# Kernel optimization log

Measured on AMD Instinct MI355X. Metric: run time of the kernel, lower is better.

The kernel has to match this reference:

```python
import jax, jax.numpy as jnp
import numpy as np

LN_EPS = 1e-5

def _cell(x, h, c, Wih, Whh, bih, bhh):
    # PyTorch LSTMCell: gate order i, f, g, o
    z = x @ Wih.T + h @ Whh.T + bih + bhh
    i, f, g, o = jnp.split(z, 4, axis=-1)
    c = jax.nn.sigmoid(f) * c + jax.nn.sigmoid(i) * jnp.tanh(g)
    h = jax.nn.sigmoid(o) * jnp.tanh(c)
    return h, c

def _forward(encoder_inputs, decoder_inputs, enc_Wih, enc_Whh, enc_bih, enc_bhh,
             dec_Wih, dec_Whh, dec_bih, dec_bhh, attn_in_w, attn_in_b,
             attn_out_w, attn_out_b, ln_g, ln_b, out_w, out_b):
    B = encoder_inputs.shape[0]
    H = enc_Whh.shape[1]
    Sd = decoder_inputs.shape[1]
    h0 = jnp.zeros((B, H), encoder_inputs.dtype)
    c0 = jnp.zeros((B, H), encoder_inputs.dtype)

    def enc_step(carry, x_t):
        h, c = _cell(x_t, carry[0], carry[1], enc_Wih, enc_Whh, enc_bih, enc_bhh)
        return (h, c), h

    (h_e, c_e), hs = jax.lax.scan(enc_step, (h0, c0), jnp.swapaxes(encoder_inputs, 0, 1))
    enc_out = jnp.swapaxes(hs, 0, 1)  # [B, Se, H]

    # MultiheadAttention (1 head): precompute K, V once since keys/values are static
    Wq, Wk, Wv = jnp.split(attn_in_w, 3, axis=0)
    bq, bk, bv = jnp.split(attn_in_b, 3)
    K = enc_out @ Wk.T + bk  # [B, Se, H]
    V = enc_out @ Wv.T + bv  # [B, Se, H]
    scale = 1.0 / float(np.sqrt(H))

    def dec_step(carry, _):
        h, c, x = carry
        h, c = _cell(x, h, c, dec_Wih, dec_Whh, dec_bih, dec_bhh)
        q = h @ Wq.T + bq  # [B, H], single query per step
        attn = jax.nn.softmax(jnp.einsum('bh,bsh->bs', q, K) * scale, axis=-1)
        ctx = jnp.einsum('bs,bsh->bh', attn, V) @ attn_out_w.T + attn_out_b
        y = ctx + h  # residual with raw (pre-projection) query, as in the torch code
        mu = jnp.mean(y, axis=-1, keepdims=True)
        var = jnp.mean((y - mu) ** 2, axis=-1, keepdims=True)
        y = (y - mu) * jax.lax.rsqrt(var + LN_EPS) * ln_g + ln_b
        out = y @ out_w.T + out_b  # [B, 1]
        return (h, c, out), out

    init = (h_e, c_e, decoder_inputs[:, 0, :])
    _, outs = jax.lax.scan(dec_step, init, None, length=Sd)
    return jnp.swapaxes(outs, 0, 1)  # [B, Sd, 1]

def setup_inputs():
    key = jax.random.key(0)
    ks = jax.random.split(key, 13)
    B, Se, Sd, H, O = 64, 512, 128, 512, 1
    s = 1.0 / float(np.sqrt(H))
    def p(k, shape, sc):
        return (jax.random.uniform(k, shape, jnp.float32) * 2.0 - 1.0) * sc
    return {
        "encoder_inputs": jax.random.normal(ks[0], (B, Se, 1), jnp.float32),
        "decoder_inputs": jax.random.normal(ks[1], (B, Sd, 1), jnp.float32),
        "enc_Wih": p(ks[2], (4 * H, 1), s), "enc_Whh": p(ks[3], (4 * H, H), s),
        "enc_bih": p(ks[4], (4 * H,), s), "enc_bhh": p(ks[5], (4 * H,), s),
        "dec_Wih": p(ks[6], (4 * H, 1), s), "dec_Whh": p(ks[7], (4 * H, H), s),
        "dec_bih": p(ks[8], (4 * H,), s), "dec_bhh": p(ks[9], (4 * H,), s),
        "attn_in_w": p(ks[10], (3 * H, H), s),
        "attn_in_b": jnp.zeros((3 * H,), jnp.float32),
        "attn_out_w": p(ks[11], (H, H), s),
        "attn_out_b": jnp.zeros((H,), jnp.float32),
        "ln_g": jnp.ones((H,), jnp.float32), "ln_b": jnp.zeros((H,), jnp.float32),
        "out_w": p(ks[12], (O, H), s), "out_b": jnp.zeros((O,), jnp.float32),
    }

def reference(encoder_inputs, decoder_inputs, enc_Wih, enc_Whh, enc_bih, enc_bhh,
              dec_Wih, dec_Whh, dec_bih, dec_bhh, attn_in_w, attn_in_b,
              attn_out_w, attn_out_b, ln_g, ln_b, out_w, out_b):
    return _forward(encoder_inputs, decoder_inputs, enc_Wih, enc_Whh, enc_bih, enc_bhh,
                    dec_Wih, dec_Whh, dec_bih, dec_bhh, attn_in_w, attn_in_b,
                    attn_out_w, attn_out_b, ln_g, ln_b, out_w, out_b)
```

## Files before the change

### kernel.cpp

```cpp
#include <hip/hip_runtime.h>
#include <hip/hip_bf16.h>
#include <stdint.h>


#define HID 512
#define NBAT 64
#define SEQE 512
#define SEQD 128
#define NGRP 4
#define GBAT 16
#define GBLK 64
#define NH 8
#define SCALE 0.04419417382415922f
#define FLS 16

typedef __attribute__((ext_vector_type(8))) short bf16x8;
typedef __attribute__((ext_vector_type(4))) float f32x4;
#define MFMA_B16 __builtin_amdgcn_mfma_f32_16x16x32_bf16

static constexpr size_t OFF_G   = 0;
static constexpr size_t OFF_NM  = OFF_G  + (size_t)HID*HID*4;
static constexpr size_t OFF_M0  = OFF_NM + (size_t)HID*HID*4;
static constexpr size_t OFF_N0  = OFF_M0 + 2048;
static constexpr size_t OFF_WQB = OFF_N0 + 2048;
static constexpr size_t OFF_SC  = OFF_WQB + 2048;
static constexpr size_t OFF_HB  = OFF_SC + 256;
static constexpr size_t OFF_CB  = OFF_HB + (size_t)3*NBAT*HID*4;
static constexpr size_t OFF_EBP = OFF_CB + (size_t)NBAT*HID*4;
static constexpr size_t OFF_MD  = OFF_EBP + (size_t)NBAT*4*HID*4;
static constexpr size_t OFF_KB  = OFF_MD + (size_t)NBAT*4*4;
static constexpr size_t OFF_FLG = OFF_KB + (size_t)NBAT*SEQE*4;
static constexpr size_t OFF_XPK = OFF_FLG + (size_t)3*NGRP*GBLK*FLS*4;
static constexpr size_t OFF_BFK = ((OFF_XPK + 512 + 255) & ~(size_t)255);
static constexpr size_t OFF_BFV = OFF_BFK + (size_t)16*32*64*8*2;
static constexpr size_t OFF_EO  = OFF_BFV + (size_t)16*32*64*8*2;
static constexpr size_t OFF_VT  = OFF_EO + (size_t)NBAT*SEQE*HID*2;

__device__ __forceinline__ float bf2f(uint32_t u) {
  union { float f; uint32_t i; } x; x.i = u << 16; return x.f;
}
__device__ __forceinline__ unsigned short bfbits(float f) {
  __hip_bfloat16 h = __float2bfloat16(f);
  return *(unsigned short*)&h;
}
__device__ __forceinline__ uint32_t splitbf(float f) {
  unsigned short hi = bfbits(f);
  union { uint32_t u; float ff; } c; c.u = (uint32_t)hi << 16;
  unsigned short lo = bfbits(f - c.ff);
  return (uint32_t)hi | ((uint32_t)lo << 16);
}
__device__ __forceinline__ float sigm(float x) { return 1.f / (1.f + __expf(-x)); }

__device__ __forceinline__ void stg(float* p, float v) {
  __hip_atomic_store(p, v, __ATOMIC_RELAXED, __HIP_MEMORY_SCOPE_AGENT);
}
__device__ __forceinline__ void stgu(uint32_t* p, uint32_t v) {
  __hip_atomic_store(p, v, __ATOMIC_RELAXED, __HIP_MEMORY_SCOPE_AGENT);
}
__device__ __forceinline__ void stgi(int* p, int v) {
  __hip_atomic_store(p, v, __ATOMIC_RELAXED, __HIP_MEMORY_SCOPE_AGENT);
}
__device__ __forceinline__ void stg64(unsigned long long* p, unsigned long long v) {
  __hip_atomic_store(p, v, __ATOMIC_RELAXED, __HIP_MEMORY_SCOPE_AGENT);
}
__device__ __forceinline__ float ldg1(const float* p) {
  return __hip_atomic_load((float*)p, __ATOMIC_RELAXED, __HIP_MEMORY_SCOPE_AGENT);
}
__device__ __forceinline__ int ldgi(const int* p) {
  return __hip_atomic_load((int*)p, __ATOMIC_RELAXED, __HIP_MEMORY_SCOPE_AGENT);
}
__device__ __forceinline__ unsigned long long ldg8(const void* p) {
  return __hip_atomic_load((unsigned long long*)p, __ATOMIC_RELAXED, __HIP_MEMORY_SCOPE_AGENT);
}

#define POLL_GE(addr, thr) \
  while (ldgi(addr) < (thr)) __builtin_amdgcn_s_sleep(1);
#define CFENCE() __asm__ __volatile__("" ::: "memory")

__global__ __launch_bounds__(256) void k0_prep(
    const float* __restrict__ aiw, const float* __restrict__ aib,
    const float* __restrict__ aow, const float* __restrict__ aob,
    const float* __restrict__ outw, const float* __restrict__ lng,
    const float* __restrict__ lnb, char* __restrict__ ws) {
  float* Gm = (float*)(ws + OFF_G);
  float* Nm = (float*)(ws + OFF_NM);
  float* m0 = (float*)(ws + OFF_M0);
  float* n0 = (float*)(ws + OFF_N0);
  float* wqb = (float*)(ws + OFF_WQB);
  float* sc = (float*)(ws + OFF_SC);
  const int blk = blockIdx.x, tid = threadIdx.x;
  if (blk == 512) {
    uint32_t* hb = (uint32_t*)(ws + OFF_HB);
    int* fl = (int*)(ws + OFF_FLG);
    unsigned long long* xpk = (unsigned long long*)(ws + OFF_XPK);
    for (int i = tid; i < 3*NBAT*HID; i += 256) hb[i] = 0u;
    for (int i = tid; i < 3*NGRP*GBLK*FLS; i += 256) fl[i] = 0;
    for (int i = tid; i < NBAT; i += 256) xpk[i] = 0ull;
    for (int l = tid; l < HID; l += 256) {
      float s = 0.f;
      for (int i = 0; i < HID; i++) s += aib[i] * aiw[(size_t)(HID + i)*HID + l];
      m0[l] = s;
    }
    for (int l = tid; l < HID; l += 256) {
      float s = 0.f;
      for (int i = 0; i < HID; i++) s += aiw[(size_t)i*HID + l] * aib[HID + i];
      wqb[l] = s;
    }
    for (int j = tid; j < HID; j += 256) {
      float s = aob[j];
      for (int i = 0; i < HID; i++) s += aow[(size_t)j*HID + i] * aib[2*HID + i];
      n0[j] = s;
    }
    __shared__ float red[256];
    float a = 0.f, b = 0.f, d = 0.f;
    for (int l = tid; l < HID; l += 256) {
      a += outw[l]*lng[l]; b += outw[l]*lnb[l]; d += aib[l]*aib[HID + l];
    }
    red[tid] = a; __syncthreads();
    for (int st = 128; st; st >>= 1) { if (tid < st) red[tid] += red[tid + st]; __syncthreads(); }
    if (tid == 0) sc[0] = red[0];
    __syncthreads();
    red[tid] = b; __syncthreads();
    for (int st = 128; st; st >>= 1) { if (tid < st) red[tid] += red[tid + st]; __syncthreads(); }
    if (tid == 0) sc[1] = red[0];
    __syncthreads();
    red[tid] = d; __syncthreads();
    for (int st = 128; st; st >>= 1) { if (tid < st) red[tid] += red[tid + st]; __syncthreads(); }
    if (tid == 0) sc[2] = red[0];
    return;
  }
  const bool isG = blk < 256;
  const int tb = isG ? blk : blk - 256;
  const int r0 = (tb >> 4) * 32, c0 = (tb & 15) * 32;
  __shared__ float sa[32][33], sb[32][33];
  float acc[4] = {0.f, 0.f, 0.f, 0.f};
  const int tr = tid >> 3, tc = (tid & 7) * 4;
  for (int i0 = 0; i0 < HID; i0 += 32) {
    __syncthreads();
    if (isG) {
      for (int j = 0; j < 4; j++) sa[tr][tc + j] = aiw[(size_t)(HID + i0 + tr)*HID + r0 + tc + j];
      for (int j = 0; j < 4; j++) sb[tr][tc + j] = aiw[(size_t)(i0 + tr)*HID + c0 + tc + j];
    } else {
      for (int j = 0; j < 4; j++) sa[tr][tc + j] = aow[(size_t)(r0 + tr)*HID + i0 + tc + j];
      for (int j = 0; j < 4; j++) sb[tr][tc + j] = aiw[(size_t)(2*HID + i0 + tr)*HID + c0 + tc + j];
    }
    __syncthreads();
    if (isG) {
      for (int i = 0; i < 32; i++) {
        float a = sa[i][tr];
        for (int j = 0; j < 4; j++) acc[j] += a * sb[i][tc + j];
      }
    } else {
      for (int i = 0; i < 32; i++) {
        float a = sa[tr][i];
        for (int j = 0; j < 4; j++) acc[j] += a * sb[i][tc + j];
      }
    }
  }
  float* dst = isG ? Gm : Nm;
  for (int j = 0; j < 4; j++) dst[(size_t)(r0 + tr)*HID + c0 + tc + j] = acc[j];
}

__global__ __launch_bounds__(256) void k0b_frag(char* __restrict__ ws) {
  const float* Gm = (const float*)(ws + OFF_G);
  const float* Nm = (const float*)(ws + OFF_NM);
  unsigned short* Bfk = (unsigned short*)(ws + OFF_BFK);
  unsigned short* Bfv = (unsigned short*)(ws + OFF_BFV);
  const int idx0 = blockIdx.x * 256 + threadIdx.x;
  for (int idx = idx0; idx < 16*32*64; idx += 64*256) {
    int ks = idx >> 11, lt = (idx >> 6) & 31, l = idx & 63;
    int lcol = lt*16 + (l & 15), krow = ks*32 + ((l >> 4) << 3);
    unsigned short hk[8] __attribute__((aligned(16)));
    unsigned short hv[8] __attribute__((aligned(16)));
    for (int j = 0; j < 8; j++) {
      hk[j] = bfbits(Gm[(size_t)(krow + j)*HID + lcol]);
      hv[j] = bfbits(Nm[(size_t)lcol*HID + krow + j]);
    }
    *(uint4*)(Bfk + (size_t)idx*8) = *(uint4*)hk;
    *(uint4*)(Bfv + (size_t)idx*8) = *(uint4*)hv;
  }
}

#define STAGE_FULL8(srcPTR)                                                           \
  {                                                                                   \
    const unsigned long long* _s = (const unsigned long long*)(srcPTR);               \
    unsigned long long _tm[8];                                                        \
    _Pragma("unroll") for (int r = 0; r < 8; r++) _tm[r] = ldg8(_s + tid + r*512);    \
    _Pragma("unroll") for (int r = 0; r < 8; r++) {                                   \
      int i = tid + r*512;                                                            \
      int bb_ = i >> 8, kk = (i & 255) * 2;                                           \
      unsigned long long u = _tm[r];                                                  \
      *(uint32_t*)&s_hh[bb_][kk] = (uint32_t)(u & 0xffffu) | (((uint32_t)(u >> 32) & 0xffffu) << 16); \
      *(uint32_t*)&s_hl[bb_][kk] = ((uint32_t)(u >> 16) & 0xffffu) | ((uint32_t)(u >> 48) << 16);     \
    }                                                                                 \
  }

#define STAGE_SLICE8(srcPTR)                                                          \
  {                                                                                   \
    const unsigned long long* _s = (const unsigned long long*)(srcPTR);               \
    const int _half = l >> 5, _co = wv*32 + (l & 31);                                 \
    unsigned long long _tm[8];                                                        \
    _Pragma("unroll") for (int r = 0; r < 8; r++)                                     \
      _tm[r] = ldg8(_s + (size_t)(_half*8 + r)*(HID/2) + _co);                        \
    const int kk = _co*2;                                                             \
    _Pragma("unroll") for (int r = 0; r < 8; r++) {                                   \
      unsigned long long u = _tm[r];                                                  \
      int bb_ = _half*8 + r;                                                          \
      *(uint32_t*)&s_hh[bb_][kk] = (uint32_t)(u & 0xffffu) | (((uint32_t)(u >> 32) & 0xffffu) << 16); \
      *(uint32_t*)&s_hl[bb_][kk] = ((uint32_t)(u >> 16) & 0xffffu) | ((uint32_t)(u >> 48) << 16);     \
    }                                                                                 \
  }

#define WFRAG_INIT_512()                                                              \
  for (int slot = tid; slot < 2*16*64; slot += 512) {                                 \
    int T = slot >> 10, ks = (slot >> 6) & 15, l_ = slot & 63;                        \
    int rloc = T*16 + (l_ & 15);                                                      \
    int grow = (rloc >> 3)*HID + hs + (rloc & 7);                                     \
    int ko = ks*32 + ((l_ >> 4) << 3);                                                \
    const float* wp = &whh[(size_t)grow*HID + ko];                                    \
    unsigned short hi[8] __attribute__((aligned(16)));                                \
    unsigned short lo[8] __attribute__((aligned(16)));                                \
    for (int j = 0; j < 8; j++) {                                                     \
      uint32_t u = splitbf(wp[j]);                                                    \
      hi[j] = (unsigned short)u; lo[j] = (unsigned short)(u >> 16);                   \
    }                                                                                 \
    *(uint4*)&s_wf[T][ks][l_][0] = *(uint4*)hi;                                       \
    *(uint4*)&s_wl[T][ks][l_][0] = *(uint4*)lo;                                       \
  }

#define CELL_MFMA8()                                                                  \
  {                                                                                   \
    f32x4 acc0 = {0.f,0.f,0.f,0.f}, acc1 = {0.f,0.f,0.f,0.f};                         \
    _Pragma("unroll") for (int kq = 0; kq < 2; kq++) {                                \
      const int ks = wv*2 + kq;                                                       \
      const int ko = ks*32 + (oc << 3);                                               \
      bf16x8 ahi = *(const bf16x8*)&s_hh[lm][ko];                                     \
      bf16x8 alo = *(const bf16x8*)&s_hl[lm][ko];                                     \
      bf16x8 b0h = *(const bf16x8*)&s_wf[0][ks][l][0];                                \
      bf16x8 b0l = *(const bf16x8*)&s_wl[0][ks][l][0];                                \
      bf16x8 b1h = *(const bf16x8*)&s_wf[1][ks][l][0];                                \
      bf16x8 b1l = *(const bf16x8*)&s_wl[1][ks][l][0];                                \
      acc0 = MFMA_B16(ahi, b0h, acc0, 0, 0, 0);                                       \
      acc0 = MFMA_B16(alo, b0h, acc0, 0, 0, 0);                                       \
      acc0 = MFMA_B16(ahi, b0l, acc0, 0, 0, 0);                                       \
      acc1 = MFMA_B16(ahi, b1h, acc1, 0, 0, 0);                                       \
      acc1 = MFMA_B16(alo, b1h, acc1, 0, 0, 0);                                       \
      acc1 = MFMA_B16(ahi, b1l, acc1, 0, 0, 0);                                       \
    }                                                                                 \
    _Pragma("unroll") for (int q = 0; q < 4; q++) {                                   \
      int idx = (oc*4 + q)*16 + lm;                                                   \
      s_pacc[wv][0][idx] = acc0[q];                                                   \
      s_pacc[wv][1][idx] = acc1[q];                                                   \
    }                                                                                 \
  }                                                                                   \
  __syncthreads();

#define CELL_MFMA8R()                                                                 \
  {                                                                                   \
    f32x4 acc0 = {0.f,0.f,0.f,0.f}, acc1 = {0.f,0.f,0.f,0.f};                         \
    _Pragma("unroll") for (int kq = 0; kq < 2; kq++) {                                \
      const int ks = wv*2 + kq;                                                       \
      const int ko = ks*32 + (oc << 3);                                               \
      bf16x8 ahi = *(const bf16x8*)&s_hh[lm][ko];                                     \
      bf16x8 alo = *(const bf16x8*)&s_hl[lm][ko];                                     \
      acc0 = MFMA_B16(ahi, wh0[kq], acc0, 0, 0, 0);                                   \
      acc0 = MFMA_B16(alo, wh0[kq], acc0, 0, 0, 0);                                   \
      acc0 = MFMA_B16(ahi, wl0[kq], acc0, 0, 0, 0);                                   \
      acc1 = MFMA_B16(ahi, wh1[kq], acc1, 0, 0, 0);                                   \
      acc1 = MFMA_B16(alo, wh1[kq], acc1, 0, 0, 0);                                   \
      acc1 = MFMA_B16(ahi, wl1[kq], acc1, 0, 0, 0);                                   \
    }                                                                                 \
    _Pragma("unroll") for (int q = 0; q < 4; q++) {                                   \
      int idx = (oc*4 + q)*16 + lm;                                                   \
      s_pacc[wv][0][idx] = acc0[q];                                                   \
      s_pacc[wv][1][idx] = acc1[q];                                                   \
    }                                                                                 \
  }                                                                                   \
  __syncthreads();

#define GATES_SUM()                                                                   \
      float zi = 0.f, zf = 0.f, zg = 0.f, zo = 0.f;                                   \
      _Pragma("unroll") for (int w = 0; w < 8; w++) {                                 \
        zi += s_pacc[w][0][b*16+j];                                                   \
        zf += s_pacc[w][0][b*16+8+j];                                                 \
        zg += s_pacc[w][1][b*16+j];                                                   \
        zo += s_pacc[w][1][b*16+8+j];                                                 \
      }                                                                               \
      float x = s_x[b];                                                               \
      zi += x*s_wih[j]    + s_bias[j];                                                \
      zf += x*s_wih[8+j]  + s_bias[8+j];                                              \
      zg += x*s_wih[16+j] + s_bias[16+j];                                             \
      zo += x*s_wih[24+j] + s_bias[24+j];

__global__ __launch_bounds__(512) void k1_enc(
    const float* __restrict__ xin, const float* __restrict__ wih,
    const float* __restrict__ whh, const float* __restrict__ bih,
    const float* __restrict__ bhh, char* __restrict__ ws) {
  const int bk = blockIdx.x, tid = threadIdx.x;
  const int g = bk >> 6, jb = bk & 63;
  const int hs = jb * NH, b0 = g * GBAT;
  uint32_t* hbuf = (uint32_t*)(ws + OFF_HB);
  float* cbuf = (float*)(ws + OFF_CB);
  unsigned short* eo = (unsigned short*)(ws + OFF_EO);
  int* fl = (int*)(ws + OFF_FLG) + g * GBLK * FLS;

  __shared__ __align__(16) unsigned short s_wf[2][16][64][8];
  __shared__ __align__(16) unsigned short s_wl[2][16][64][8];
  __shared__ __align__(16) unsigned short s_hh[GBAT][520];
  __shared__ __align__(16) unsigned short s_hl[GBAT][520];
  __shared__ float s_pacc[8][2][256];
  __shared__ float s_c[GBAT][NH];
  __shared__ float s_x[GBAT];
  __shared__ float s_wih[32], s_bias[32];

  WFRAG_INIT_512()
  if (tid < 32) {
    int grow = (tid >> 3)*HID + hs + (tid & 7);
    s_wih[tid] = wih[grow];
    s_bias[tid] = bih[grow] + bhh[grow];
  }
  for (int i = tid; i < GBAT*NH; i += 512) s_c[i >> 3][i & 7] = 0.f;
  __syncthreads();

  const int l = tid & 63, wv = tid >> 6;
  const int lm = l & 15, oc = l >> 4;

  for (int t = 0; t < SEQE; t++) {
    if (tid < GBAT) s_x[tid] = xin[(size_t)(b0 + tid)*SEQE + t];
    if (l < 8) { POLL_GE(&fl[(wv*8 + l)*FLS], t) }
    CFENCE();
    STAGE_SLICE8(hbuf + (size_t)(t % 3)*NBAT*HID + (size_t)b0*HID)
    CELL_MFMA8()
    if (tid < 128) {
      int b = tid >> 3, j = tid & 7;
      GATES_SUM()
      float c = s_c[b][j];
      c = sigm(zf)*c + sigm(zi)*tanhf(zg);
      float hv = sigm(zo)*tanhf(c);
      s_c[b][j] = c;
      uint32_t pk = splitbf(hv);
      stgu(&hbuf[(size_t)((t+1)%3)*NBAT*HID + (size_t)(b0+b)*HID + hs + j], pk);
      eo[((size_t)(b0+b)*SEQE + t)*HID + hs + j] = (unsigned short)(pk & 0xffffu);
    }
    __syncthreads();
    if (tid == 0) stgi(&fl[jb*FLS], t + 1);
  }
  __syncthreads();
  if (tid < GBAT*NH)
    cbuf[(size_t)(b0 + (tid >> 3))*HID + hs + (tid & 7)] = s_c[tid >> 3][tid & 7];
}

__global__ __launch_bounds__(256) void k0c_kv(char* __restrict__ ws) {
  const float* wqb = (const float*)(ws + OFF_WQB);
  const float* m0 = (const float*)(ws + OFF_M0);
  const float* scv = (const float*)(ws + OFF_SC);
  const unsigned short* Bfk = (const unsigned short*)(ws + OFF_BFK);
  const unsigned short* Bfv = (const unsigned short*)(ws + OFF_BFV);
  unsigned short* eoK = (unsigned short*)(ws + OFF_EO);
  unsigned short* Vt = (unsigned short*)(ws + OFF_VT);
  float* kbv = (float*)(ws + OFF_KB);
  const int b = blockIdx.x >> 4, s0 = (blockIdx.x & 15) * 32;
  const int tid = threadIdx.x;
  __shared__ __align__(16) unsigned short s_e[32][520];
  __shared__ float s_kb[32][8];
  {
    const uint4* src = (const uint4*)(eoK + ((size_t)b*SEQE + s0)*HID);
    #pragma unroll
    for (int r = 0; r < 8; r++) {
      int i = tid + r*256;
      uint4 v = src[i];
      int rr = i >> 6, cc = (i & 63)*8;
      *(uint4*)&s_e[rr][cc] = v;
    }
  }
  __syncthreads();
  const int l = tid & 63, wv = tid >> 6, lm = l & 15, oc = l >> 4;
  for (int nt = 0; nt < 8; nt++) {
    const int lt = wv*8 + nt;
    f32x4 accK0 = {0,0,0,0}, accK1 = {0,0,0,0}, accV0 = {0,0,0,0}, accV1 = {0,0,0,0};
    #pragma unroll
    for (int ks = 0; ks < 16; ks++) {
      bf16x8 yk = *(const bf16x8*)(Bfk + (((size_t)ks*32 + lt)*64 + l)*8);
      bf16x8 yv = *(const bf16x8*)(Bfv + (((size_t)ks*32 + lt)*64 + l)*8);
      bf16x8 xe0 = *(const bf16x8*)&s_e[lm][ks*32 + oc*8];
      bf16x8 xe1 = *(const bf16x8*)&s_e[16 + lm][ks*32 + oc*8];
      accK0 = MFMA_B16(xe0, yk, accK0, 0,0,0);
      accK1 = MFMA_B16(xe1, yk, accK1, 0,0,0);
      accV0 = MFMA_B16(xe0, yv, accV0, 0,0,0);
      accV1 = MFMA_B16(xe1, yv, accV1, 0,0,0);
    }
    const float wq = wqb[lt*16 + lm];
    #pragma unroll
    for (int st = 0; st < 2; st++) {
      const f32x4& aK = st ? accK1 : accK0;
      const f32x4& aV = st ? accV1 : accV0;
      #pragma unroll
      for (int q = 0; q < 4; q++)
        eoK[((size_t)b*SEQE + s0 + st*16 + oc*4 + q)*HID + lt*16 + lm] = bfbits(aK[q] + wq);
      unsigned short pv[4] __attribute__((aligned(8)));
      #pragma unroll
      for (int q = 0; q < 4; q++) pv[q] = bfbits(aV[q]);
      *(unsigned long long*)(Vt + ((size_t)b*HID + lt*16 + lm)*SEQE + s0 + st*16 + oc*4)
          = *(unsigned long long*)pv;
    }
  }
  {
    int s = tid >> 3, kc = tid & 7;
    float acc = 0.f;
    for (int i = 0; i < 64; i++) {
      int k = kc*64 + i;
      acc += bf2f((uint32_t)s_e[s][k]) * m0[k];
    }
    s_kb[s][kc] = acc;
  }
  __syncthreads();
  if (tid < 32) {
    float a = 0.f;
    for (int kc = 0; kc < 8; kc++) a += s_kb[tid][kc];
    kbv[(size_t)b*SEQE + s0 + tid] = a + scv[2];
  }
}

__global__ __launch_bounds__(512) void k2_dec(
    const float* __restrict__ xin, const float* __restrict__ wih,
    const float* __restrict__ whh, const float* __restrict__ bih,
    const float* __restrict__ bhh, const float* __restrict__ lng,
    const float* __restrict__ lnb, const float* __restrict__ outw,
    const float* __restrict__ outb, char* __restrict__ ws,
    float* __restrict__ dout) {
  const int bk = blockIdx.x, tid = threadIdx.x;
  const int g = bk >> 6, jb = bk & 63;
  const int hs = jb * NH, b0 = g * GBAT;
  uint32_t* hbuf = (uint32_t*)(ws + OFF_HB);
  float* cbuf = (float*)(ws + OFF_CB);
  float* ebp  = (float*)(ws + OFF_EBP);
  float* md   = (float*)(ws + OFF_MD);
  const float* n0v = (const float*)(ws + OFF_N0);
  const float* scv = (const float*)(ws + OFF_SC);
  const float* kbv = (const float*)(ws + OFF_KB);
  const unsigned short* Kt = (const unsigned short*)(ws + OFF_EO);
  const unsigned short* Vt = (const unsigned short*)(ws + OFF_VT);
  unsigned long long* xpk = (unsigned long long*)(ws + OFF_XPK);
  int* fl2 = (int*)(ws + OFF_FLG) + (NGRP + g) * GBLK * FLS;
  int* pfl = (int*)(ws + OFF_FLG) + (2*NGRP + g) * GBLK * FLS;

  __shared__ __align__(16) unsigned short s_hh[GBAT][520];
  __shared__ __align__(16) unsigned short s_hl[GBAT][520];
  __shared__ __align__(16) unsigned short s_kt[64][520];
  __shared__ float s_pacc[8][2][256];
  __shared__ float s_c[GBAT][NH];
  __shared__ float s_x[GBAT];
  __shared__ float s_wih[32], s_bias[32];
  __shared__ float s_scores[128];
  __shared__ __align__(16) uint32_t s_pbf[64];
  __shared__ float s_red[32];
  __shared__ float s_ln[HID], s_n0f[HID];

  const int l = tid & 63, wv = tid >> 6;
  const int lm = l & 15, oc = l >> 4;
  const int bb = jb >> 2, scq = jb & 3, batch = b0 + bb;

  bf16x8 wh0[2], wl0[2], wh1[2], wl1[2];
  #pragma unroll
  for (int kq = 0; kq < 2; kq++) {
    const int ks = wv*2 + kq;
    #pragma unroll
    for (int T = 0; T < 2; T++) {
      int rloc = T*16 + lm;
      int grow = (rloc >> 3)*HID + hs + (rloc & 7);
      const float* wp = &whh[(size_t)grow*HID + ks*32 + oc*8];
      unsigned short hi8[8] __attribute__((aligned(16)));
      unsigned short lo8[8] __attribute__((aligned(16)));
      #pragma unroll
      for (int j = 0; j < 8; j++) {
        uint32_t u = splitbf(wp[j]);
        hi8[j] = (unsigned short)u; lo8[j] = (unsigned short)(u >> 16);
      }
      if (T == 0) { wh0[kq] = *(bf16x8*)hi8; wl0[kq] = *(bf16x8*)lo8; }
      else        { wh1[kq] = *(bf16x8*)hi8; wl1[kq] = *(bf16x8*)lo8; }
    }
  }
  bf16x8 vreg[4][4];
  {
    const unsigned short* vp = Vt + (size_t)batch*HID*SEQE + (size_t)scq*128;
    #pragma unroll
    for (int n = 0; n < 4; n++)
      #pragma unroll
      for (int ks = 0; ks < 4; ks++)
        vreg[n][ks] = *(const bf16x8*)(vp + (size_t)((wv*4 + n)*16 + lm)*SEQE + ks*32 + oc*8);
  }
  for (int i = tid; i < 4096; i += 512) {
    int row = i >> 6, cc = (i & 63) * 8;
    *(uint4*)&s_kt[row][cc] =
        *(const uint4*)(Kt + ((size_t)batch*SEQE + scq*128 + row)*HID + cc);
  }
  if (tid < 32) {
    int grow = (tid >> 3)*HID + hs + (tid & 7);
    s_wih[tid] = wih[grow];
    s_bias[tid] = bih[grow] + bhh[grow];
  }
  for (int i = tid; i < HID; i += 512) {
    s_ln[i] = outw[i] * lng[i];
    s_n0f[i] = n0v[i];
  }
  for (int i = tid; i < GBAT*NH; i += 512)
    s_c[i >> 3][i & 7] = cbuf[(size_t)(b0 + (i >> 3))*HID + hs + (i & 7)];
  const float Swg = scv[0], Swb = scv[1], ob0 = outb[0];

  STAGE_FULL8(hbuf + (size_t)2*NBAT*HID + (size_t)b0*HID)
  if (tid < GBAT) s_x[tid] = xin[(size_t)(b0 + tid)*SEQD];
  __syncthreads();

  for (int t = 0; t < SEQD; t++) {
    CELL_MFMA8R()
    if (tid < 128) {
      int b = tid >> 3, j = tid & 7;
      GATES_SUM()
      float c = s_c[b][j];
      c = sigm(zf)*c + sigm(zi)*tanhf(zg);
      float hv = sigm(zo)*tanhf(c);
      s_c[b][j] = c;
      stgu(&hbuf[(size_t)((t+1)%3)*NBAT*HID + (size_t)(b0+b)*HID + hs + j], splitbf(hv));
    }
    __syncthreads();
    if (tid == 0) stgi(&fl2[jb*FLS], t + 1);
    if (l < 8) { POLL_GE(&fl2[(wv*8 + l)*FLS], t + 1) }
    CFENCE();
    STAGE_SLICE8(hbuf + (size_t)((t+1)%3)*NBAT*HID + (size_t)b0*HID)
    __syncthreads();
    {
      f32x4 acc = {0.f,0.f,0.f,0.f};
      if (wv < 4) {
        #pragma unroll
        for (int ks = 0; ks < 16; ks++) {
          bf16x8 xh = *(const bf16x8*)&s_hh[bb][ks*32 + oc*8];
          bf16x8 yk = *(const bf16x8*)&s_kt[wv*16 + lm][ks*32 + oc*8];
          acc = MFMA_B16(xh, yk, acc, 0, 0, 0);
        }
      } else {
        const unsigned short* kp =
            Kt + ((size_t)batch*SEQE + scq*128 + 64 + (wv - 4)*16)*HID;
        #pragma unroll
        for (int ks = 0; ks < 16; ks++) {
          bf16x8 xh = *(const bf16x8*)&s_hh[bb][ks*32 + oc*8];
          bf16x8 yk = *(const bf16x8*)(kp + (size_t)lm*HID + ks*32 + oc*8);
          acc = MFMA_B16(xh, yk, acc, 0, 0, 0);
        }
      }
      if (oc == 0) s_scores[wv*16 + lm] = acc[0];
    }
    __syncthreads();
    float den_part = 0.f;
    if (tid < 128) {
      float sv = (s_scores[tid] + kbv[(size_t)batch*SEQE + scq*128 + tid]) * SCALE;
      den_part = __expf(sv);
      s_scores[tid] = den_part;
    }
    __syncthreads();
    if (tid < 64)
      s_pbf[tid] = (uint32_t)bfbits(s_scores[2*tid]) | ((uint32_t)bfbits(s_scores[2*tid+1]) << 16);
    if (tid < 128) {
      for (int off = 32; off; off >>= 1) den_part += __shfl_down(den_part, off);
      if ((tid & 63) == 0) s_red[tid >> 6] = den_part;
    }
    __syncthreads();
    if (tid == 0) stg(&md[batch*4 + scq], s_red[0] + s_red[1]);
    {
      #pragma unroll
      for (int n = 0; n < 4; n++) {
        const int lv0 = (wv*4 + n)*16;
        f32x4 acc = {0.f,0.f,0.f,0.f};
        #pragma unroll
        for (int ks = 0; ks < 4; ks++) {
          bf16x8 xp = *(const bf16x8*)((const unsigned short*)s_pbf + ks*32 + oc*8);
          acc = MFMA_B16(xp, vreg[n][ks], acc, 0, 0, 0);
        }
        if (oc == 0) stg(&ebp[((size_t)batch*4 + scq)*HID + lv0 + lm], acc[0]);
      }
    }
    __syncthreads();
    if (tid == 0) stgi(&pfl[jb*FLS], t + 1);
    if (jb < GBAT) {
      #pragma unroll
      for (int q = 0; q < 4; q++) { POLL_GE(&pfl[(4*jb + q)*FLS], t + 1) }
      CFENCE();
      const int mb = b0 + jb;
      if (tid < 4) s_red[tid] = ldg1(&md[mb*4 + tid]);
      __syncthreads();
      const float inv = 1.f / (s_red[0] + s_red[1] + s_red[2] + s_red[3]);
      if (tid < 256) {
        float sy = 0.f, sy2 = 0.f, sg = 0.f;
        #pragma unroll
        for (int u = 0; u < 2; u++) {
          const int lv = tid*2 + u;
          float p0 = ldg1(&ebp[((size_t)mb*4 + 0)*HID + lv]);
          float p1 = ldg1(&ebp[((size_t)mb*4 + 1)*HID + lv]);
          float p2 = ldg1(&ebp[((size_t)mb*4 + 2)*HID + lv]);
          float p3 = ldg1(&ebp[((size_t)mb*4 + 3)*HID + lv]);
          float hval = bf2f((uint32_t)s_hh[jb][lv]) + bf2f((uint32_t)s_hl[jb][lv]);
          float y = (p0 + p1 + p2 + p3)*inv + s_n0f[lv] + hval;
          sy += y; sy2 += y*y; sg += s_ln[lv]*y;
        }
        for (int off = 32; off; off >>= 1) {
          sy += __shfl_down(sy, off); sy2 += __shfl_down(sy2, off); sg += __shfl_down(sg, off);
        }
        if (l == 0) { s_red[8+wv] = sy; s_red[12+wv] = sy2; s_red[16+wv] = sg; }
      }
      __syncthreads();
      if (tid == 0) {
        float Sy  = s_red[8]  + s_red[9]  + s_red[10] + s_red[11];
        float Sy2 = s_red[12] + s_red[13] + s_red[14] + s_red[15];
        float Sg  = s_red[16] + s_red[17] + s_red[18] + s_red[19];
        float mu = Sy * (1.f/HID);
        float var = Sy2 * (1.f/HID) - mu*mu;
        float rs = rsqrtf(var + 1e-5f);
        float o = rs*(Sg - mu*Swg) + Swb + ob0;
        dout[(size_t)mb*SEQD + t] = o;
        union { float f; uint32_t u; } cv; cv.f = o;
        stg64(&xpk[mb], ((unsigned long long)cv.u << 32) | (uint32_t)(t + 1));
      }
    }
    if (tid < GBAT) {
      unsigned long long v;
      do { v = ldg8(&xpk[b0 + tid]); __builtin_amdgcn_s_sleep(1); }
      while ((uint32_t)v < (uint32_t)(t + 1));
      union { uint32_t u; float f; } cv; cv.u = (uint32_t)(v >> 32);
      s_x[tid] = cv.f;
    }
    CFENCE();
  }
}

extern "C" void kernel_launch(void* const* d_in, const int* in_sizes, int n_in,
                              void* d_out, int out_size, void* d_ws, size_t ws_size,
                              hipStream_t stream) {
  const float* enc_in = (const float*)d_in[0];
  const float* dec_in = (const float*)d_in[1];
  const float* ewih = (const float*)d_in[2];
  const float* ewhh = (const float*)d_in[3];
  const float* ebih = (const float*)d_in[4];
  const float* ebhh = (const float*)d_in[5];
  const float* dwih = (const float*)d_in[6];
  const float* dwhh = (const float*)d_in[7];
  const float* dbih = (const float*)d_in[8];
  const float* dbhh = (const float*)d_in[9];
  const float* aiw  = (const float*)d_in[10];
  const float* aib  = (const float*)d_in[11];
  const float* aow  = (const float*)d_in[12];
  const float* aob  = (const float*)d_in[13];
  const float* lng  = (const float*)d_in[14];
  const float* lnb  = (const float*)d_in[15];
  const float* outw = (const float*)d_in[16];
  const float* outb = (const float*)d_in[17];
  char* ws = (char*)d_ws;
  k0_prep<<<513, 256, 0, stream>>>(aiw, aib, aow, aob, outw, lng, lnb, ws);
  k0b_frag<<<64, 256, 0, stream>>>(ws);
  k1_enc<<<256, 512, 0, stream>>>(enc_in, ewih, ewhh, ebih, ebhh, ws);
  k0c_kv<<<1024, 256, 0, stream>>>(ws);
  k2_dec<<<256, 512, 0, stream>>>(dec_in, dwih, dwhh, dbih, dbhh,
                                  lng, lnb, outw, outb, ws, (float*)d_out);
}
```

Measured before the change: 2.832 ms.

## Finalize output in owning block, defer x poll past recurrent MFMA

The LayerNorm/output step for each batch now runs in the block with scq==0, which already holds one of the four partial attention sums and its softmax denominator in shared memory. It reads only the other three partials from global memory and polls three flags instead of four. The wait for the previous step's output x moves to after the recurrent h·Whh MFMA, so that matmul overlaps the cross-block dependency instead of stalling at the end of the iteration. This adds a __syncthreads per step and a 2 KB shared buffer, and it relies on CELL_MFMA8R not reading s_x.

```diff
diff --git a/kernel.cpp b/kernel.cpp
--- a/kernel.cpp
+++ b/kernel.cpp
@@ -448,6 +448,8 @@
   __shared__ __align__(16) unsigned short s_hl[GBAT][520];
   __shared__ __align__(16) unsigned short s_kt[64][520];
   __shared__ float s_pacc[8][2][256];
+  __shared__ float s_own[HID];
+  __shared__ float s_d0;
   __shared__ float s_c[GBAT][NH];
   __shared__ float s_x[GBAT];
   __shared__ float s_wih[32], s_bias[32];
@@ -513,6 +515,16 @@
 
   for (int t = 0; t < SEQD; t++) {
     CELL_MFMA8R()
+    if (t > 0) {
+      if (tid < GBAT) {
+        unsigned long long v;
+        do { v = ldg8(&xpk[b0 + tid]); __builtin_amdgcn_s_sleep(1); }
+        while ((uint32_t)v < (uint32_t)t);
+        union { uint32_t u; float f; } cv; cv.u = (uint32_t)(v >> 32);
+        s_x[tid] = cv.f;
+      }
+      __syncthreads();
+    }
     if (tid < 128) {
       int b = tid >> 3, j = tid & 7;
       GATES_SUM()
@@ -564,7 +576,11 @@
       if ((tid & 63) == 0) s_red[tid >> 6] = den_part;
     }
     __syncthreads();
-    if (tid == 0) stg(&md[batch*4 + scq], s_red[0] + s_red[1]);
+    if (tid == 0) {
+      float den = s_red[0] + s_red[1];
+      stg(&md[batch*4 + scq], den);
+      s_d0 = den;
+    }
     {
       #pragma unroll
       for (int n = 0; n < 4; n++) {
@@ -575,29 +591,32 @@
           bf16x8 xp = *(const bf16x8*)((const unsigned short*)s_pbf + ks*32 + oc*8);
           acc = MFMA_B16(xp, vreg[n][ks], acc, 0, 0, 0);
         }
-        if (oc == 0) stg(&ebp[((size_t)batch*4 + scq)*HID + lv0 + lm], acc[0]);
+        if (oc == 0) {
+          stg(&ebp[((size_t)batch*4 + scq)*HID + lv0 + lm], acc[0]);
+          s_own[lv0 + lm] = acc[0];
+        }
       }
     }
     __syncthreads();
     if (tid == 0) stgi(&pfl[jb*FLS], t + 1);
-    if (jb < GBAT) {
+    if (scq == 0) {
+      const int mb = batch;
       #pragma unroll
-      for (int q = 0; q < 4; q++) { POLL_GE(&pfl[(4*jb + q)*FLS], t + 1) }
+      for (int q = 1; q < 4; q++) { POLL_GE(&pfl[(4*bb + q)*FLS], t + 1) }
       CFENCE();
-      const int mb = b0 + jb;
-      if (tid < 4) s_red[tid] = ldg1(&md[mb*4 + tid]);
+      if (tid < 3) s_red[tid] = ldg1(&md[mb*4 + 1 + tid]);
       __syncthreads();
-      const float inv = 1.f / (s_red[0] + s_red[1] + s_red[2] + s_red[3]);
+      const float inv = 1.f / (s_d0 + s_red[0] + s_red[1] + s_red[2]);
       if (tid < 256) {
         float sy = 0.f, sy2 = 0.f, sg = 0.f;
         #pragma unroll
         for (int u = 0; u < 2; u++) {
           const int lv = tid*2 + u;
-          float p0 = ldg1(&ebp[((size_t)mb*4 + 0)*HID + lv]);
+          float p0 = s_own[lv];
           float p1 = ldg1(&ebp[((size_t)mb*4 + 1)*HID + lv]);
           float p2 = ldg1(&ebp[((size_t)mb*4 + 2)*HID + lv]);
           float p3 = ldg1(&ebp[((size_t)mb*4 + 3)*HID + lv]);
-          float hval = bf2f((uint32_t)s_hh[jb][lv]) + bf2f((uint32_t)s_hl[jb][lv]);
+          float hval = bf2f((uint32_t)s_hh[bb][lv]) + bf2f((uint32_t)s_hl[bb][lv]);
           float y = (p0 + p1 + p2 + p3)*inv + s_n0f[lv] + hval;
           sy += y; sy2 += y*y; sg += s_ln[lv]*y;
         }
@@ -620,14 +639,6 @@
         stg64(&xpk[mb], ((unsigned long long)cv.u << 32) | (uint32_t)(t + 1));
       }
     }
-    if (tid < GBAT) {
-      unsigned long long v;
-      do { v = ldg8(&xpk[b0 + tid]); __builtin_amdgcn_s_sleep(1); }
-      while ((uint32_t)v < (uint32_t)(t + 1));
-      union { uint32_t u; float f; } cv; cv.u = (uint32_t)(v >> 32);
-      s_x[tid] = cv.f;
-    }
-    CFENCE();
   }
 }
 
```

After: 2.659 ms. 1.07x faster.
